# Kernel optimization log

Measured on AMD Instinct MI355X. Metric: run time of the kernel, lower is better.

Reference implementation:

```python
import jax, jax.numpy as jnp
import numpy as np

D_MODEL = 1024
N_HEADS = 16
N_GROUPS = 4
D_FF = 4096
N_EXPERTS = 8
TOP_K = 2
BATCH = 2
SEQ = 1024
D_K = D_MODEL // N_HEADS
HPG = N_HEADS // N_GROUPS
EPS = 1e-6


def rms_norm(x, w):
    rms = jnp.sqrt(jnp.mean(x * x, axis=-1, keepdims=True) + EPS)
    return x / rms * w


def rope(x):
    # RoPE over FULL d_model, halves concatenated (faithful to source quirk)
    d = x.shape[-1]
    half = d // 2
    theta = 1.0 / (10000.0 ** (jnp.arange(half, dtype=jnp.float32) / half))
    pos = jnp.arange(x.shape[1], dtype=jnp.float32)[:, None]  # [S,1]
    ang = pos * theta[None, :]                                 # [S,half]
    cos, sin = jnp.cos(ang), jnp.sin(ang)
    xe, xo = x[..., 0::2], x[..., 1::2]
    return jnp.concatenate([xe * cos - xo * sin, xe * sin + xo * cos], axis=-1)


def attention(x, Wq, Wk, Wv, Wo):
    B, S, _ = x.shape
    xr = rope(x)
    Q = (xr @ Wq).reshape(B, S, N_HEADS, D_K).transpose(0, 2, 1, 3)  # [B,H,S,dk]
    Q = Q.reshape(B, N_GROUPS, HPG, S, D_K)
    K = (xr @ Wk).reshape(B, S, N_GROUPS, D_K).transpose(0, 2, 1, 3)  # [B,G,S,dk]
    V = (xr @ Wv).reshape(B, S, N_GROUPS, D_K).transpose(0, 2, 1, 3)
    scores = jnp.einsum('bghsd,bgtd->bghst', Q, K) / jnp.sqrt(jnp.float32(D_K))
    mask = jnp.triu(jnp.full((S, S), -1e9, dtype=scores.dtype), k=1)
    attn = jax.nn.softmax(scores + mask, axis=-1)
    out = jnp.einsum('bghst,bgtd->bghsd', attn, V)            # [B,G,Hg,S,dv]
    out = out.reshape(B, N_HEADS, S, D_K).transpose(0, 2, 1, 3).reshape(B, S, D_MODEL)
    return out @ Wo


def moe(x, router_w, router_b, W1, b1, W2, b2, W3, b3):
    B, S, _ = x.shape
    logits = x @ router_w + router_b                          # [B,S,E]
    topv, topi = jax.lax.top_k(logits, TOP_K)                 # [B,S,K]
    topw = jax.nn.softmax(topv, axis=-1)                      # [B,S,K]
    # scatter top-k weights into dense [B,S,E] combine matrix
    onehot = jax.nn.one_hot(topi, N_EXPERTS, dtype=x.dtype)   # [B,S,K,E]
    comb = jnp.einsum('bsk,bske->bse', topw, onehot)          # [B,S,E]
    # dense all-expert SwiGLU (same math as per-token dispatch loop)
    h1 = jnp.einsum('bsd,edf->ebsf', x, W1) + b1[:, None, None, :]
    h2 = jnp.einsum('bsd,edf->ebsf', x, W2) + b2[:, None, None, :]
    h = h2 * jax.nn.silu(h1)
    eo = jnp.einsum('ebsf,efd->ebsd', h, W3) + b3[:, None, None, :]
    return jnp.einsum('bse,ebsd->bsd', comb, eo)


def setup_inputs() -> dict:
    key = jax.random.key(0)
    ks = jax.random.split(key, 16)
    s = 0.02
    return {
        'x': jax.random.normal(ks[0], (BATCH, SEQ, D_MODEL), dtype=jnp.float32),
        'norm1_w': jnp.ones((D_MODEL,), jnp.float32),
        'Wq': jax.random.normal(ks[1], (D_MODEL, D_MODEL), jnp.float32) * s,
        'Wk': jax.random.normal(ks[2], (D_MODEL, N_GROUPS * D_K), jnp.float32) * s,
        'Wv': jax.random.normal(ks[3], (D_MODEL, N_GROUPS * D_K), jnp.float32) * s,
        'Wo': jax.random.normal(ks[4], (D_MODEL, D_MODEL), jnp.float32) * s,
        'norm2_w': jnp.ones((D_MODEL,), jnp.float32),
        'router_w': jax.random.normal(ks[5], (D_MODEL, N_EXPERTS), jnp.float32) * s,
        'router_b': jnp.zeros((N_EXPERTS,), jnp.float32),
        'W1': jax.random.normal(ks[6], (N_EXPERTS, D_MODEL, D_FF), jnp.float32) * s,
        'b1': jnp.zeros((N_EXPERTS, D_FF), jnp.float32),
        'W2': jax.random.normal(ks[7], (N_EXPERTS, D_MODEL, D_FF), jnp.float32) * s,
        'b2': jnp.zeros((N_EXPERTS, D_FF), jnp.float32),
        'W3': jax.random.normal(ks[8], (N_EXPERTS, D_FF, D_MODEL), jnp.float32) * s,
        'b3': jnp.zeros((N_EXPERTS, D_MODEL), jnp.float32),
    }


def reference(x, norm1_w, Wq, Wk, Wv, Wo, norm2_w, router_w, router_b,
              W1, b1, W2, b2, W3, b3):
    h = x + attention(rms_norm(x, norm1_w), Wq, Wk, Wv, Wo)
    h = h + moe(rms_norm(h, norm2_w), router_w, router_b, W1, b1, W2, b2, W3, b3)
    return h
```

## Files before the change

kernel.cpp:

```cpp
#include <hip/hip_runtime.h>

#define D_MODEL 1024
#define N_HEADS 16
#define N_GROUPS 4
#define D_FF 4096
#define N_EXPERTS 8
#define BATCH 2
#define SEQ 1024
#define DK 64
#define NTOK (BATCH*SEQ)
#define KVD (N_GROUPS*DK)
#define QKVN (D_MODEL + 2*KVD)
#define APAD 72

typedef unsigned short u16;
typedef unsigned int u32;
typedef __attribute__((ext_vector_type(8))) short short8;
typedef __attribute__((ext_vector_type(8))) __bf16 bf16x8;
typedef __attribute__((ext_vector_type(4))) float floatx4;

__device__ __forceinline__ float bf2f(u16 s){ return __uint_as_float(((u32)s)<<16); }
__device__ __forceinline__ u16 f2bf(float f){
  u32 u = __float_as_uint(f);
  u += 0x7fffu + ((u>>16)&1u);
  return (u16)(u>>16);
}
__device__ __forceinline__ floatx4 mfma16(short8 a, short8 b, floatx4 c){
  return __builtin_amdgcn_mfma_f32_16x16x32_bf16(
      __builtin_bit_cast(bf16x8, a), __builtin_bit_cast(bf16x8, b), c, 0, 0, 0);
}
__device__ __forceinline__ void gload16(const u16* g, u16* l){
  __builtin_amdgcn_global_load_lds(
      (const __attribute__((address_space(1))) u32*)g,
      (__attribute__((address_space(3))) u32*)l, 16, 0, 0);
}

__global__ __launch_bounds__(256) void k_cvt_t(
    const float* __restrict__ src, u16* __restrict__ dst, int K, int N)
{
  size_t moff = (size_t)blockIdx.z * K * N;
  src += moff; dst += moff;
  int k0 = blockIdx.y*64, n0 = blockIdx.x*64;
  __shared__ __align__(16) u16 t[64*72];
  int tid = threadIdx.x;
  #pragma unroll
  for (int i=0;i<4;i++){
    int idx = i*256 + tid;
    int r = idx>>4;
    int c = (idx&15)*4;
    float4 v = *(const float4*)(src + (size_t)(k0+r)*N + n0 + c);
    t[(c+0)*72 + r] = f2bf(v.x);
    t[(c+1)*72 + r] = f2bf(v.y);
    t[(c+2)*72 + r] = f2bf(v.z);
    t[(c+3)*72 + r] = f2bf(v.w);
  }
  __syncthreads();
  #pragma unroll
  for (int i=0;i<2;i++){
    int idx = i*256 + tid;
    int n = idx>>3;
    int kc = (idx&7)*8;
    *(uint4*)(dst + (size_t)(n0+n)*K + k0 + kc) = *(const uint4*)&t[n*72 + kc];
  }
}

__global__ __launch_bounds__(256) void k_rmsnorm_rope(
    const float* __restrict__ x, const float* __restrict__ w, u16* __restrict__ xr)
{
  int tok = blockIdx.x;
  int s = tok & (SEQ-1);
  int tid = threadIdx.x;
  const float* xrow = x + (size_t)tok * D_MODEL;
  __shared__ float red[256];
  float4 v = ((const float4*)xrow)[tid];
  red[tid] = v.x*v.x + v.y*v.y + v.z*v.z + v.w*v.w;
  __syncthreads();
  for (int o=128;o>0;o>>=1){ if(tid<o) red[tid]+=red[tid+o]; __syncthreads(); }
  float inv = rsqrtf(red[0]*(1.0f/D_MODEL) + 1e-6f);
  u16* orow = xr + (size_t)tok * D_MODEL;
  #pragma unroll
  for (int ii=0; ii<2; ii++){
    int i = tid + ii*256;
    float2 p = ((const float2*)xrow)[i];
    float2 wp = ((const float2*)w)[i];
    float xe = p.x*inv*wp.x;
    float xo = p.y*inv*wp.y;
    float th = __expf(-(float)i * (9.210340371976184f/512.0f));
    float ang = (float)s * th;
    float c = cosf(ang), sn = sinf(ang);
    orow[i]       = f2bf(xe*c - xo*sn);
    orow[i+512]   = f2bf(xe*sn + xo*c);
  }
}

__global__ __launch_bounds__(256) void k_gemm_t(
    const u16* __restrict__ A, const u16* __restrict__ Bt,
    u16* __restrict__ C, int M, int N, int K)
{
  __shared__ __align__(16) u16 As[128*32];
  __shared__ __align__(16) u16 Bs[128*32];
  int tid = threadIdx.x;
  int wave = tid>>6, lane = tid&63, l15 = lane&15, q = lane>>4;
  int wm = wave>>1, wn = wave&1;
  int m0 = blockIdx.y*128, n0 = blockIdx.x*128;
  const u16* ap0 = A  + (size_t)(m0 + (tid>>2))*K + (tid&3)*8;
  const u16* ap1 = ap0 + (size_t)64*K;
  const u16* bp0 = Bt + (size_t)(n0 + (tid>>2))*K + (tid&3)*8;
  const u16* bp1 = bp0 + (size_t)64*K;
  u16* asb0 = As + wave*512;
  u16* asb1 = As + 2048 + wave*512;
  u16* bsb0 = Bs + wave*512;
  u16* bsb1 = Bs + 2048 + wave*512;
  floatx4 acc[4][4];
  #pragma unroll
  for (int i=0;i<4;i++)
    #pragma unroll
    for (int j=0;j<4;j++) acc[i][j] = (floatx4){0.f,0.f,0.f,0.f};
  for (int k0=0;k0<K;k0+=32){
    __syncthreads();
    gload16(ap0 + k0, asb0);
    gload16(ap1 + k0, asb1);
    gload16(bp0 + k0, bsb0);
    gload16(bp1 + k0, bsb1);
    __syncthreads();
    short8 af[4], bf[4];
    #pragma unroll
    for (int i=0;i<4;i++) af[i] = *(const short8*)&As[(wm*64 + i*16 + l15)*32 + q*8];
    #pragma unroll
    for (int i=0;i<4;i++) bf[i] = *(const short8*)&Bs[(wn*64 + i*16 + l15)*32 + q*8];
    #pragma unroll
    for (int mi=0;mi<4;mi++)
      #pragma unroll
      for (int ni=0;ni<4;ni++)
        acc[mi][ni] = mfma16(af[mi], bf[ni], acc[mi][ni]);
  }
  #pragma unroll
  for (int mi=0;mi<4;mi++)
    #pragma unroll
    for (int ni=0;ni<4;ni++)
      #pragma unroll
      for (int r=0;r<4;r++){
        int row = m0 + wm*64 + mi*16 + q*4 + r;
        int col = n0 + wn*64 + ni*16 + l15;
        C[(size_t)row*N + col] = f2bf(acc[mi][ni][r]);
      }
}

__global__ __launch_bounds__(256) void k_gemm_resid(
    const u16* __restrict__ A, const u16* __restrict__ Bt,
    const float* __restrict__ resid, float* __restrict__ hacc,
    float* __restrict__ out, int M, int N, int K)
{
  __shared__ __align__(16) u16 As[128*32];
  __shared__ __align__(16) u16 Bs[128*32];
  int tid = threadIdx.x;
  int wave = tid>>6, lane = tid&63, l15 = lane&15, q = lane>>4;
  int wm = wave>>1, wn = wave&1;
  int m0 = blockIdx.y*128, n0 = blockIdx.x*128;
  const u16* ap0 = A  + (size_t)(m0 + (tid>>2))*K + (tid&3)*8;
  const u16* ap1 = ap0 + (size_t)64*K;
  const u16* bp0 = Bt + (size_t)(n0 + (tid>>2))*K + (tid&3)*8;
  const u16* bp1 = bp0 + (size_t)64*K;
  u16* asb0 = As + wave*512;
  u16* asb1 = As + 2048 + wave*512;
  u16* bsb0 = Bs + wave*512;
  u16* bsb1 = Bs + 2048 + wave*512;
  floatx4 acc[4][4];
  #pragma unroll
  for (int i=0;i<4;i++)
    #pragma unroll
    for (int j=0;j<4;j++) acc[i][j] = (floatx4){0.f,0.f,0.f,0.f};
  for (int k0=0;k0<K;k0+=32){
    __syncthreads();
    gload16(ap0 + k0, asb0);
    gload16(ap1 + k0, asb1);
    gload16(bp0 + k0, bsb0);
    gload16(bp1 + k0, bsb1);
    __syncthreads();
    short8 af[4], bf[4];
    #pragma unroll
    for (int i=0;i<4;i++) af[i] = *(const short8*)&As[(wm*64 + i*16 + l15)*32 + q*8];
    #pragma unroll
    for (int i=0;i<4;i++) bf[i] = *(const short8*)&Bs[(wn*64 + i*16 + l15)*32 + q*8];
    #pragma unroll
    for (int mi=0;mi<4;mi++)
      #pragma unroll
      for (int ni=0;ni<4;ni++)
        acc[mi][ni] = mfma16(af[mi], bf[ni], acc[mi][ni]);
  }
  #pragma unroll
  for (int mi=0;mi<4;mi++)
    #pragma unroll
    for (int ni=0;ni<4;ni++)
      #pragma unroll
      for (int r=0;r<4;r++){
        int row = m0 + wm*64 + mi*16 + q*4 + r;
        int col = n0 + wn*64 + ni*16 + l15;
        size_t idx = (size_t)row*N + col;
        float v = acc[mi][ni][r] + resid[idx];
        hacc[idx] = v;
        out[idx]  = v;
      }
}

__global__ __launch_bounds__(256) void k_vtrans(
    const u16* __restrict__ qkv, u16* __restrict__ Vt)
{
  int st = blockIdx.x;
  int bg = blockIdx.y;
  int b = bg >> 2, g = bg & 3;
  int tid = threadIdx.x;
  __shared__ u16 tile[64*APAD];
  #pragma unroll
  for (int i=0;i<2;i++){
    int idx = i*256 + tid;
    int srow = idx >> 3, cch = (idx&7)*8;
    uint4 v = *(const uint4*)(qkv + (size_t)(b*SEQ + st*64 + srow)*QKVN
                              + D_MODEL + KVD + g*64 + cch);
    *(uint4*)&tile[srow*APAD + cch] = v;
  }
  __syncthreads();
  #pragma unroll
  for (int i=0;i<2;i++){
    int idx = i*256 + tid;
    int drow = idx >> 3, sch = (idx&7)*8;
    u16 tmp[8];
    #pragma unroll
    for (int j=0;j<8;j++) tmp[j] = tile[(sch+j)*APAD + drow];
    *(uint4*)(Vt + ((size_t)(bg*64 + drow))*SEQ + st*64 + sch) = *(uint4*)tmp;
  }
}

__global__ __launch_bounds__(256) void k_attn_flash(
    const u16* __restrict__ qkv, const u16* __restrict__ Vt, u16* __restrict__ O)
{
  int qt = blockIdx.x, h = blockIdx.y, b = blockIdx.z;
  int g = h >> 2;
  int tid = threadIdx.x, wave = tid>>6, lane = tid&63, l15 = lane&15, q = lane>>4;
  __shared__ u16 Ks[64*APAD];
  __shared__ u16 Vs[64*APAD];
  __shared__ u16 Ps[4*16*APAD];

  int qbase = qt*64;
  const u16* qrow = qkv + (size_t)(b*SEQ + qbase + wave*16 + l15)*QKVN + h*64;
  short8 qa0 = *(const short8*)(qrow + q*8);
  short8 qa1 = *(const short8*)(qrow + 32 + q*8);

  floatx4 Of[4];
  #pragma unroll
  for (int nt=0;nt<4;nt++) Of[nt] = (floatx4){0.f,0.f,0.f,0.f};
  float mrun[4], lrun[4];
  #pragma unroll
  for (int r=0;r<4;r++){ mrun[r] = -1e30f; lrun[r] = 0.f; }

  for (int t=0; t<=qt; ++t){
    int kbase = t*64;
    __syncthreads();
    #pragma unroll
    for (int i=0;i<2;i++){
      int idx = i*256 + tid;
      int row = idx >> 3, cch = (idx&7)*8;
      uint4 kv = *(const uint4*)(qkv + (size_t)(b*SEQ + kbase + row)*QKVN
                                 + D_MODEL + g*64 + cch);
      *(uint4*)&Ks[row*APAD + cch] = kv;
      uint4 vv = *(const uint4*)(Vt + ((size_t)((b*4+g)*64 + row))*SEQ + kbase + cch);
      *(uint4*)&Vs[row*APAD + cch] = vv;
    }
    __syncthreads();

    floatx4 Sf[4];
    #pragma unroll
    for (int jt=0;jt<4;jt++){
      short8 bf0 = *(const short8*)&Ks[(jt*16+l15)*APAD + q*8];
      short8 bf1 = *(const short8*)&Ks[(jt*16+l15)*APAD + 32 + q*8];
      Sf[jt] = mfma16(qa0, bf0, (floatx4){0.f,0.f,0.f,0.f});
      Sf[jt] = mfma16(qa1, bf1, Sf[jt]);
    }
    bool maskt = (t == qt);
    #pragma unroll
    for (int r=0;r<4;r++){
      float s0 = Sf[0][r]*0.125f, s1 = Sf[1][r]*0.125f,
            s2 = Sf[2][r]*0.125f, s3 = Sf[3][r]*0.125f;
      if (maskt){
        int qg = qbase + wave*16 + q*4 + r;
        if (kbase +      l15 > qg) s0 = -1e30f;
        if (kbase + 16 + l15 > qg) s1 = -1e30f;
        if (kbase + 32 + l15 > qg) s2 = -1e30f;
        if (kbase + 48 + l15 > qg) s3 = -1e30f;
      }
      float mx = fmaxf(fmaxf(s0,s1), fmaxf(s2,s3));
      #pragma unroll
      for (int o=1;o<16;o<<=1) mx = fmaxf(mx, __shfl_xor(mx, o, 64));
      float mc = fmaxf(mrun[r], mx);
      float alpha = __expf(mrun[r]-mc);
      float p0 = __expf(s0-mc), p1 = __expf(s1-mc), p2 = __expf(s2-mc), p3 = __expf(s3-mc);
      float rs = p0+p1+p2+p3;
      #pragma unroll
      for (int o=1;o<16;o<<=1) rs += __shfl_xor(rs, o, 64);
      lrun[r] = lrun[r]*alpha + rs;
      mrun[r] = mc;
      #pragma unroll
      for (int nt=0;nt<4;nt++) Of[nt][r] *= alpha;
      int prow = wave*16*APAD + (q*4+r)*APAD;
      Ps[prow +      l15] = f2bf(p0);
      Ps[prow + 16 + l15] = f2bf(p1);
      Ps[prow + 32 + l15] = f2bf(p2);
      Ps[prow + 48 + l15] = f2bf(p3);
    }
    #pragma unroll
    for (int ks=0;ks<2;ks++){
      short8 pa = *(const short8*)&Ps[wave*16*APAD + l15*APAD + ks*32 + q*8];
      #pragma unroll
      for (int nt=0;nt<4;nt++){
        short8 vb = *(const short8*)&Vs[(nt*16+l15)*APAD + ks*32 + q*8];
        Of[nt] = mfma16(pa, vb, Of[nt]);
      }
    }
  }
  #pragma unroll
  for (int r=0;r<4;r++){
    float linv = 1.0f / lrun[r];
    int row = b*SEQ + qbase + wave*16 + q*4 + r;
    #pragma unroll
    for (int nt=0;nt<4;nt++){
      O[(size_t)row*D_MODEL + h*64 + nt*16 + l15] = f2bf(Of[nt][r]*linv);
    }
  }
}

__global__ __launch_bounds__(256) void k_rmsnorm2(
    const float* __restrict__ hacc, const float* __restrict__ w, u16* __restrict__ hn)
{
  int tok = blockIdx.x, tid = threadIdx.x;
  float4 v = ((const float4*)(hacc + (size_t)tok*D_MODEL))[tid];
  __shared__ float red[256];
  red[tid] = v.x*v.x + v.y*v.y + v.z*v.z + v.w*v.w;
  __syncthreads();
  for (int o=128;o>0;o>>=1){ if(tid<o) red[tid]+=red[tid+o]; __syncthreads(); }
  float inv = rsqrtf(red[0]*(1.0f/D_MODEL) + 1e-6f);
  int i = tid*4;
  float4 wv = ((const float4*)w)[tid];
  u16* orow = hn + (size_t)tok*D_MODEL;
  orow[i+0] = f2bf(v.x*inv*wv.x);
  orow[i+1] = f2bf(v.y*inv*wv.y);
  orow[i+2] = f2bf(v.z*inv*wv.z);
  orow[i+3] = f2bf(v.w*inv*wv.w);
}

__global__ __launch_bounds__(64) void k_router(
    const float* __restrict__ hacc, const float* __restrict__ w2,
    const float* __restrict__ rw, const float* __restrict__ rb,
    int* __restrict__ topi, float* __restrict__ topw)
{
  int tok = blockIdx.x, lane = threadIdx.x;
  const float* xrow = hacc + (size_t)tok*D_MODEL;
  float ss = 0.f;
  #pragma unroll
  for (int ii=0; ii<4; ii++){
    float4 v = ((const float4*)xrow)[lane + ii*64];
    ss += v.x*v.x + v.y*v.y + v.z*v.z + v.w*v.w;
  }
  #pragma unroll
  for (int o=32;o>0;o>>=1) ss += __shfl_down(ss, o, 64);
  ss = __shfl(ss, 0, 64);
  float inv = rsqrtf(ss*(1.0f/D_MODEL) + 1e-6f);
  float accv[8] = {0.f,0.f,0.f,0.f,0.f,0.f,0.f,0.f};
  for (int d = lane; d < D_MODEL; d += 64){
    float xv = xrow[d]*inv*w2[d];
    float4 r0 = ((const float4*)(rw + (size_t)d*8))[0];
    float4 r1 = ((const float4*)(rw + (size_t)d*8))[1];
    accv[0] += xv*r0.x; accv[1] += xv*r0.y;
    accv[2] += xv*r0.z; accv[3] += xv*r0.w;
    accv[4] += xv*r1.x; accv[5] += xv*r1.y;
    accv[6] += xv*r1.z; accv[7] += xv*r1.w;
  }
  #pragma unroll
  for (int e=0;e<8;e++){
    #pragma unroll
    for (int o=32;o>0;o>>=1) accv[e] += __shfl_down(accv[e], o, 64);
  }
  if (lane==0){
    float lg[8];
    #pragma unroll
    for (int e=0;e<8;e++) lg[e] = accv[e] + rb[e];
    int i0=0; float v0=lg[0];
    for (int e=1;e<8;e++) if (lg[e]>v0){v0=lg[e]; i0=e;}
    int i1=-1; float v1=-1e30f;
    for (int e=0;e<8;e++) if (e!=i0 && lg[e]>v1){v1=lg[e]; i1=e;}
    float e1 = __expf(v1-v0);
    float wsum = 1.f + e1;
    topi[tok*2+0]=i0; topi[tok*2+1]=i1;
    topw[tok*2+0]=1.f/wsum; topw[tok*2+1]=e1/wsum;
  }
}

__global__ __launch_bounds__(256) void k_pack(
    const int* __restrict__ topi, const float* __restrict__ topw,
    int* __restrict__ off, int* __restrict__ perm, float* __restrict__ pw)
{
  __shared__ int cnt[8], cur[8], offs[9];
  int tid = threadIdx.x;
  if (tid<8) cnt[tid]=0;
  __syncthreads();
  for (int i=tid;i<NTOK*2;i+=256) atomicAdd(&cnt[topi[i]],1);
  __syncthreads();
  if (tid==0){
    int s=0;
    for (int e=0;e<8;e++){ offs[e]=s; s+=cnt[e]; }
    offs[8]=s;
    for (int e=0;e<9;e++) off[e]=offs[e];
  }
  __syncthreads();
  if (tid<8) cur[tid]=offs[tid];
  __syncthreads();
  for (int i=tid;i<NTOK*2;i+=256){
    int e = topi[i];
    int pos = atomicAdd(&cur[e],1);
    perm[pos] = i>>1;
    pw[pos]   = topw[i];
  }
}

__global__ __launch_bounds__(256) void k_moe1(
    const u16* __restrict__ hn,
    const u16* __restrict__ W1t, const float* __restrict__ b1,
    const u16* __restrict__ W2t, const float* __restrict__ b2,
    const int* __restrict__ off, const int* __restrict__ perm,
    u16* __restrict__ H)
{
  int e = blockIdx.z;
  int base = off[e], cnte = off[e+1]-base;
  int mt = blockIdx.y;
  if (mt*128 >= cnte) return;
  int n0 = blockIdx.x*64;
  __shared__ __align__(16) u16 As[128*32];
  __shared__ __align__(16) u16 B1s[64*32];
  __shared__ __align__(16) u16 B2s[64*32];
  int tid = threadIdx.x;
  int wave = tid>>6, lane = tid&63, l15 = lane&15, q = lane>>4;
  int wm = wave>>1, wn = wave&1;
  int r0 = mt*128 + (tid>>2), r1 = r0 + 64;
  int t0 = (r0 < cnte) ? perm[base+r0] : 0;
  int t1 = (r1 < cnte) ? perm[base+r1] : 0;
  const u16* ap0 = hn + (size_t)t0*D_MODEL + (tid&3)*8;
  const u16* ap1 = hn + (size_t)t1*D_MODEL + (tid&3)*8;
  const u16* b1p = W1t + (size_t)e*D_FF*D_MODEL + (size_t)(n0 + (tid>>2))*D_MODEL + (tid&3)*8;
  const u16* b2p = W2t + (size_t)e*D_FF*D_MODEL + (size_t)(n0 + (tid>>2))*D_MODEL + (tid&3)*8;
  u16* asb0 = As + wave*512;
  u16* asb1 = As + 2048 + wave*512;
  u16* b1sb = B1s + wave*512;
  u16* b2sb = B2s + wave*512;
  floatx4 acc1[4][2], acc2[4][2];
  #pragma unroll
  for (int i=0;i<4;i++)
    #pragma unroll
    for (int j=0;j<2;j++){ acc1[i][j]=(floatx4){0.f,0.f,0.f,0.f}; acc2[i][j]=(floatx4){0.f,0.f,0.f,0.f}; }
  for (int k0=0;k0<D_MODEL;k0+=32){
    __syncthreads();
    gload16(ap0 + k0, asb0);
    gload16(ap1 + k0, asb1);
    gload16(b1p + k0, b1sb);
    gload16(b2p + k0, b2sb);
    __syncthreads();
    short8 af[4], f1[2], f2[2];
    #pragma unroll
    for (int i=0;i<4;i++) af[i] = *(const short8*)&As[(wm*64 + i*16 + l15)*32 + q*8];
    #pragma unroll
    for (int i=0;i<2;i++){
      f1[i] = *(const short8*)&B1s[(wn*32 + i*16 + l15)*32 + q*8];
      f2[i] = *(const short8*)&B2s[(wn*32 + i*16 + l15)*32 + q*8];
    }
    #pragma unroll
    for (int mi=0;mi<4;mi++)
      #pragma unroll
      for (int ni=0;ni<2;ni++){
        acc1[mi][ni] = mfma16(af[mi], f1[ni], acc1[mi][ni]);
        acc2[mi][ni] = mfma16(af[mi], f2[ni], acc2[mi][ni]);
      }
  }
  #pragma unroll
  for (int mi=0;mi<4;mi++)
    #pragma unroll
    for (int ni=0;ni<2;ni++)
      #pragma unroll
      for (int r=0;r<4;r++){
        int rloc = wm*64 + mi*16 + q*4 + r;
        int grow = mt*128 + rloc;
        if (grow < cnte){
          int col = n0 + wn*32 + ni*16 + l15;
          float h1 = acc1[mi][ni][r] + b1[e*D_FF+col];
          float h2 = acc2[mi][ni][r] + b2[e*D_FF+col];
          float sil = h1 / (1.f + __expf(-h1));
          H[(size_t)(base + grow)*D_FF + col] = f2bf(h2*sil);
        }
      }
}

__global__ __launch_bounds__(256) void k_moe2(
    const u16* __restrict__ H, const u16* __restrict__ W3t, const float* __restrict__ b3,
    const int* __restrict__ off, const int* __restrict__ perm, const float* __restrict__ pw,
    float* __restrict__ out)
{
  int e = blockIdx.z;
  int base = off[e], cnte = off[e+1]-base;
  int mt = blockIdx.y;
  if (mt*128 >= cnte) return;
  int n0 = blockIdx.x*128;
  __shared__ __align__(16) u16 As[128*32];
  __shared__ __align__(16) u16 Bs[128*32];
  int tid = threadIdx.x;
  int wave = tid>>6, lane = tid&63, l15 = lane&15, q = lane>>4;
  int wm = wave>>1, wn = wave&1;
  const u16* ap0 = H + (size_t)(base + mt*128 + (tid>>2))*D_FF + (tid&3)*8;
  const u16* ap1 = ap0 + (size_t)64*D_FF;
  const u16* bp0 = W3t + (size_t)e*D_MODEL*D_FF + (size_t)(n0 + (tid>>2))*D_FF + (tid&3)*8;
  const u16* bp1 = bp0 + (size_t)64*D_FF;
  u16* asb0 = As + wave*512;
  u16* asb1 = As + 2048 + wave*512;
  u16* bsb0 = Bs + wave*512;
  u16* bsb1 = Bs + 2048 + wave*512;
  floatx4 acc[4][4];
  #pragma unroll
  for (int i=0;i<4;i++)
    #pragma unroll
    for (int j=0;j<4;j++) acc[i][j] = (floatx4){0.f,0.f,0.f,0.f};
  for (int k0=0;k0<D_FF;k0+=32){
    __syncthreads();
    gload16(ap0 + k0, asb0);
    gload16(ap1 + k0, asb1);
    gload16(bp0 + k0, bsb0);
    gload16(bp1 + k0, bsb1);
    __syncthreads();
    short8 af[4], bf[4];
    #pragma unroll
    for (int i=0;i<4;i++) af[i] = *(const short8*)&As[(wm*64 + i*16 + l15)*32 + q*8];
    #pragma unroll
    for (int i=0;i<4;i++) bf[i] = *(const short8*)&Bs[(wn*64 + i*16 + l15)*32 + q*8];
    #pragma unroll
    for (int mi=0;mi<4;mi++)
      #pragma unroll
      for (int ni=0;ni<4;ni++)
        acc[mi][ni] = mfma16(af[mi], bf[ni], acc[mi][ni]);
  }
  #pragma unroll
  for (int mi=0;mi<4;mi++)
    #pragma unroll
    for (int ni=0;ni<4;ni++)
      #pragma unroll
      for (int r=0;r<4;r++){
        int grow = mt*128 + wm*64 + mi*16 + q*4 + r;
        if (grow < cnte){
          int col = n0 + wn*64 + ni*16 + l15;
          int tok = perm[base+grow];
          float wgt = pw[base+grow];
          float val = acc[mi][ni][r] + b3[e*D_MODEL+col];
          atomicAdd(out + (size_t)tok*D_MODEL + col, wgt*val);
        }
      }
}

extern "C" void kernel_launch(void* const* d_in, const int* in_sizes, int n_in,
                              void* d_out, int out_size, void* d_ws, size_t ws_size,
                              hipStream_t stream)
{
  const float* x   = (const float*)d_in[0];
  const float* n1w = (const float*)d_in[1];
  const float* Wq  = (const float*)d_in[2];
  const float* Wk  = (const float*)d_in[3];
  const float* Wv  = (const float*)d_in[4];
  const float* Wo  = (const float*)d_in[5];
  const float* n2w = (const float*)d_in[6];
  const float* rw  = (const float*)d_in[7];
  const float* rb  = (const float*)d_in[8];
  const float* W1  = (const float*)d_in[9];
  const float* b1  = (const float*)d_in[10];
  const float* W2  = (const float*)d_in[11];
  const float* b2  = (const float*)d_in[12];
  const float* W3  = (const float*)d_in[13];
  const float* b3  = (const float*)d_in[14];
  float* out = (float*)d_out;

  char* p = (char*)d_ws;
  auto alloc = [&](size_t bytes)->char*{
    char* r = p; p += (bytes + 255) & ~(size_t)255; return r;
  };
  u16*   xr   = (u16*)  alloc((size_t)NTOK*D_MODEL*2);
  u16*   qkv  = (u16*)  alloc((size_t)NTOK*QKVN*2);
  u16*   Vt   = (u16*)  alloc((size_t)NTOK*KVD*2);
  u16*   attn = (u16*)  alloc((size_t)NTOK*D_MODEL*2);
  u16*   hn   = (u16*)  alloc((size_t)NTOK*D_MODEL*2);
  float* acc  = (float*)alloc((size_t)NTOK*D_MODEL*4);
  int*   topi = (int*)  alloc((size_t)NTOK*2*4);
  float* topw = (float*)alloc((size_t)NTOK*2*4);
  int*   off  = (int*)  alloc(64);
  int*   perm = (int*)  alloc((size_t)NTOK*2*4);
  float* pw   = (float*)alloc((size_t)NTOK*2*4);
  u16*   H    = (u16*)  alloc((size_t)NTOK*2*D_FF*2);
  u16*   Wqkvt= (u16*)  alloc((size_t)QKVN*D_MODEL*2);
  u16*   Wot  = (u16*)  alloc((size_t)D_MODEL*D_MODEL*2);
  u16*   W1t  = (u16*)  alloc((size_t)N_EXPERTS*D_MODEL*D_FF*2);
  u16*   W2t  = (u16*)  alloc((size_t)N_EXPERTS*D_MODEL*D_FF*2);
  u16*   W3t  = (u16*)  alloc((size_t)N_EXPERTS*D_FF*D_MODEL*2);

  k_cvt_t<<<dim3(D_MODEL/64, D_MODEL/64, 1), 256, 0, stream>>>(Wq, Wqkvt, D_MODEL, D_MODEL);
  k_cvt_t<<<dim3(KVD/64,     D_MODEL/64, 1), 256, 0, stream>>>(Wk, Wqkvt + (size_t)D_MODEL*D_MODEL, D_MODEL, KVD);
  k_cvt_t<<<dim3(KVD/64,     D_MODEL/64, 1), 256, 0, stream>>>(Wv, Wqkvt + (size_t)(D_MODEL+KVD)*D_MODEL, D_MODEL, KVD);
  k_cvt_t<<<dim3(D_MODEL/64, D_MODEL/64, 1), 256, 0, stream>>>(Wo, Wot, D_MODEL, D_MODEL);
  k_cvt_t<<<dim3(D_FF/64,    D_MODEL/64, N_EXPERTS), 256, 0, stream>>>(W1, W1t, D_MODEL, D_FF);
  k_cvt_t<<<dim3(D_FF/64,    D_MODEL/64, N_EXPERTS), 256, 0, stream>>>(W2, W2t, D_MODEL, D_FF);
  k_cvt_t<<<dim3(D_MODEL/64, D_FF/64,    N_EXPERTS), 256, 0, stream>>>(W3, W3t, D_FF, D_MODEL);

  k_rmsnorm_rope<<<NTOK, 256, 0, stream>>>(x, n1w, xr);
  k_gemm_t<<<dim3(QKVN/128, NTOK/128), 256, 0, stream>>>(xr, Wqkvt, qkv, NTOK, QKVN, D_MODEL);
  k_vtrans<<<dim3(SEQ/64, BATCH*N_GROUPS), 256, 0, stream>>>(qkv, Vt);
  k_attn_flash<<<dim3(SEQ/64, N_HEADS, BATCH), 256, 0, stream>>>(qkv, Vt, attn);
  k_gemm_resid<<<dim3(D_MODEL/128, NTOK/128), 256, 0, stream>>>(attn, Wot, x, acc, out, NTOK, D_MODEL, D_MODEL);
  k_rmsnorm2<<<NTOK, 256, 0, stream>>>(acc, n2w, hn);
  k_router<<<NTOK, 64, 0, stream>>>(acc, n2w, rw, rb, topi, topw);
  k_pack<<<1, 256, 0, stream>>>(topi, topw, off, perm, pw);
  k_moe1<<<dim3(D_FF/64,    32, N_EXPERTS), 256, 0, stream>>>(hn, W1t, b1, W2t, b2, off, perm, H);
  k_moe2<<<dim3(D_MODEL/128, 32, N_EXPERTS), 256, 0, stream>>>(H, W3t, b3, off, perm, pw, out);
}
```

Baseline: 843.2 us.

## Double-buffer LDS in GEMM kernels, shrink M tiles, split-K the MoE down projection

Adds a two-stage LDS ping-pong to the QKV, output-projection and both MoE GEMMs, so the global load for the next K slice is issued before the MFMAs on the current slice and one barrier per iteration is dropped. The dense GEMMs and moe2 move from 128-row to 64-row M tiles to launch more blocks, and moe2 splits K in two, with both halves accumulating through the existing atomics and the bias added only once. The cost is twice the shared memory per block, which may lower occupancy, less reuse per tile, and twice as many atomic adds into the output in moe2.

```diff
diff --git a/kernel.cpp b/kernel.cpp
--- a/kernel.cpp
+++ b/kernel.cpp
@@ -97,50 +97,50 @@
     const u16* __restrict__ A, const u16* __restrict__ Bt,
     u16* __restrict__ C, int M, int N, int K)
 {
-  __shared__ __align__(16) u16 As[128*32];
-  __shared__ __align__(16) u16 Bs[128*32];
+  __shared__ __align__(16) u16 As[2][64*32];
+  __shared__ __align__(16) u16 Bs[2][128*32];
   int tid = threadIdx.x;
   int wave = tid>>6, lane = tid&63, l15 = lane&15, q = lane>>4;
   int wm = wave>>1, wn = wave&1;
-  int m0 = blockIdx.y*128, n0 = blockIdx.x*128;
-  const u16* ap0 = A  + (size_t)(m0 + (tid>>2))*K + (tid&3)*8;
-  const u16* ap1 = ap0 + (size_t)64*K;
+  int m0 = blockIdx.y*64, n0 = blockIdx.x*128;
+  const u16* ap  = A  + (size_t)(m0 + (tid>>2))*K + (tid&3)*8;
   const u16* bp0 = Bt + (size_t)(n0 + (tid>>2))*K + (tid&3)*8;
   const u16* bp1 = bp0 + (size_t)64*K;
-  u16* asb0 = As + wave*512;
-  u16* asb1 = As + 2048 + wave*512;
-  u16* bsb0 = Bs + wave*512;
-  u16* bsb1 = Bs + 2048 + wave*512;
-  floatx4 acc[4][4];
-  #pragma unroll
-  for (int i=0;i<4;i++)
+  auto stage = [&](int buf, int k){
+    gload16(ap  + k, &As[buf][wave*512]);
+    gload16(bp0 + k, &Bs[buf][wave*512]);
+    gload16(bp1 + k, &Bs[buf][2048 + wave*512]);
+  };
+  floatx4 acc[2][4];
+  #pragma unroll
+  for (int i=0;i<2;i++)
     #pragma unroll
     for (int j=0;j<4;j++) acc[i][j] = (floatx4){0.f,0.f,0.f,0.f};
-  for (int k0=0;k0<K;k0+=32){
-    __syncthreads();
-    gload16(ap0 + k0, asb0);
-    gload16(ap1 + k0, asb1);
-    gload16(bp0 + k0, bsb0);
-    gload16(bp1 + k0, bsb1);
-    __syncthreads();
-    short8 af[4], bf[4];
-    #pragma unroll
-    for (int i=0;i<4;i++) af[i] = *(const short8*)&As[(wm*64 + i*16 + l15)*32 + q*8];
-    #pragma unroll
-    for (int i=0;i<4;i++) bf[i] = *(const short8*)&Bs[(wn*64 + i*16 + l15)*32 + q*8];
-    #pragma unroll
-    for (int mi=0;mi<4;mi++)
+  int NS = K/32, cur = 0;
+  stage(0, 0);
+  __syncthreads();
+  for (int ks=0; ks<NS; ++ks){
+    if (ks+1 < NS) stage(cur^1, (ks+1)*32);
+    short8 af[2], bf[4];
+    #pragma unroll
+    for (int i=0;i<2;i++) af[i] = *(const short8*)&As[cur][(wm*32 + i*16 + l15)*32 + q*8];
+    #pragma unroll
+    for (int i=0;i<4;i++) bf[i] = *(const short8*)&Bs[cur][(wn*64 + i*16 + l15)*32 + q*8];
+    #pragma unroll
+    for (int mi=0;mi<2;mi++)
       #pragma unroll
       for (int ni=0;ni<4;ni++)
         acc[mi][ni] = mfma16(af[mi], bf[ni], acc[mi][ni]);
-  }
-  #pragma unroll
-  for (int mi=0;mi<4;mi++)
+    __syncthreads();
+    cur ^= 1;
+  }
+  #pragma unroll
+  for (int mi=0;mi<2;mi++)
     #pragma unroll
     for (int ni=0;ni<4;ni++)
       #pragma unroll
       for (int r=0;r<4;r++){
-        int row = m0 + wm*64 + mi*16 + q*4 + r;
+        int row = m0 + wm*32 + mi*16 + q*4 + r;
         int col = n0 + wn*64 + ni*16 + l15;
         C[(size_t)row*N + col] = f2bf(acc[mi][ni][r]);
       }
@@ -151,50 +151,50 @@
     const float* __restrict__ resid, float* __restrict__ hacc,
     float* __restrict__ out, int M, int N, int K)
 {
-  __shared__ __align__(16) u16 As[128*32];
-  __shared__ __align__(16) u16 Bs[128*32];
+  __shared__ __align__(16) u16 As[2][64*32];
+  __shared__ __align__(16) u16 Bs[2][128*32];
   int tid = threadIdx.x;
   int wave = tid>>6, lane = tid&63, l15 = lane&15, q = lane>>4;
   int wm = wave>>1, wn = wave&1;
-  int m0 = blockIdx.y*128, n0 = blockIdx.x*128;
-  const u16* ap0 = A  + (size_t)(m0 + (tid>>2))*K + (tid&3)*8;
-  const u16* ap1 = ap0 + (size_t)64*K;
+  int m0 = blockIdx.y*64, n0 = blockIdx.x*128;
+  const u16* ap  = A  + (size_t)(m0 + (tid>>2))*K + (tid&3)*8;
   const u16* bp0 = Bt + (size_t)(n0 + (tid>>2))*K + (tid&3)*8;
   const u16* bp1 = bp0 + (size_t)64*K;
-  u16* asb0 = As + wave*512;
-  u16* asb1 = As + 2048 + wave*512;
-  u16* bsb0 = Bs + wave*512;
-  u16* bsb1 = Bs + 2048 + wave*512;
-  floatx4 acc[4][4];
-  #pragma unroll
-  for (int i=0;i<4;i++)
+  auto stage = [&](int buf, int k){
+    gload16(ap  + k, &As[buf][wave*512]);
+    gload16(bp0 + k, &Bs[buf][wave*512]);
+    gload16(bp1 + k, &Bs[buf][2048 + wave*512]);
+  };
+  floatx4 acc[2][4];
+  #pragma unroll
+  for (int i=0;i<2;i++)
     #pragma unroll
     for (int j=0;j<4;j++) acc[i][j] = (floatx4){0.f,0.f,0.f,0.f};
-  for (int k0=0;k0<K;k0+=32){
-    __syncthreads();
-    gload16(ap0 + k0, asb0);
-    gload16(ap1 + k0, asb1);
-    gload16(bp0 + k0, bsb0);
-    gload16(bp1 + k0, bsb1);
-    __syncthreads();
-    short8 af[4], bf[4];
-    #pragma unroll
-    for (int i=0;i<4;i++) af[i] = *(const short8*)&As[(wm*64 + i*16 + l15)*32 + q*8];
-    #pragma unroll
-    for (int i=0;i<4;i++) bf[i] = *(const short8*)&Bs[(wn*64 + i*16 + l15)*32 + q*8];
-    #pragma unroll
-    for (int mi=0;mi<4;mi++)
+  int NS = K/32, cur = 0;
+  stage(0, 0);
+  __syncthreads();
+  for (int ks=0; ks<NS; ++ks){
+    if (ks+1 < NS) stage(cur^1, (ks+1)*32);
+    short8 af[2], bf[4];
+    #pragma unroll
+    for (int i=0;i<2;i++) af[i] = *(const short8*)&As[cur][(wm*32 + i*16 + l15)*32 + q*8];
+    #pragma unroll
+    for (int i=0;i<4;i++) bf[i] = *(const short8*)&Bs[cur][(wn*64 + i*16 + l15)*32 + q*8];
+    #pragma unroll
+    for (int mi=0;mi<2;mi++)
       #pragma unroll
       for (int ni=0;ni<4;ni++)
         acc[mi][ni] = mfma16(af[mi], bf[ni], acc[mi][ni]);
-  }
-  #pragma unroll
-  for (int mi=0;mi<4;mi++)
+    __syncthreads();
+    cur ^= 1;
+  }
+  #pragma unroll
+  for (int mi=0;mi<2;mi++)
     #pragma unroll
     for (int ni=0;ni<4;ni++)
       #pragma unroll
       for (int r=0;r<4;r++){
-        int row = m0 + wm*64 + mi*16 + q*4 + r;
+        int row = m0 + wm*32 + mi*16 + q*4 + r;
         int col = n0 + wn*64 + ni*16 + l15;
         size_t idx = (size_t)row*N + col;
         float v = acc[mi][ni][r] + resid[idx];
@@ -433,9 +433,9 @@
   int mt = blockIdx.y;
   if (mt*128 >= cnte) return;
   int n0 = blockIdx.x*64;
-  __shared__ __align__(16) u16 As[128*32];
-  __shared__ __align__(16) u16 B1s[64*32];
-  __shared__ __align__(16) u16 B2s[64*32];
+  __shared__ __align__(16) u16 As[2][128*32];
+  __shared__ __align__(16) u16 B1s[2][64*32];
+  __shared__ __align__(16) u16 B2s[2][64*32];
   int tid = threadIdx.x;
   int wave = tid>>6, lane = tid&63, l15 = lane&15, q = lane>>4;
   int wm = wave>>1, wn = wave&1;
@@ -446,29 +446,29 @@
   const u16* ap1 = hn + (size_t)t1*D_MODEL + (tid&3)*8;
   const u16* b1p = W1t + (size_t)e*D_FF*D_MODEL + (size_t)(n0 + (tid>>2))*D_MODEL + (tid&3)*8;
   const u16* b2p = W2t + (size_t)e*D_FF*D_MODEL + (size_t)(n0 + (tid>>2))*D_MODEL + (tid&3)*8;
-  u16* asb0 = As + wave*512;
-  u16* asb1 = As + 2048 + wave*512;
-  u16* b1sb = B1s + wave*512;
-  u16* b2sb = B2s + wave*512;
+  auto stage = [&](int buf, int k){
+    gload16(ap0 + k, &As[buf][wave*512]);
+    gload16(ap1 + k, &As[buf][2048 + wave*512]);
+    gload16(b1p + k, &B1s[buf][wave*512]);
+    gload16(b2p + k, &B2s[buf][wave*512]);
+  };
   floatx4 acc1[4][2], acc2[4][2];
   #pragma unroll
   for (int i=0;i<4;i++)
     #pragma unroll
     for (int j=0;j<2;j++){ acc1[i][j]=(floatx4){0.f,0.f,0.f,0.f}; acc2[i][j]=(floatx4){0.f,0.f,0.f,0.f}; }
-  for (int k0=0;k0<D_MODEL;k0+=32){
-    __syncthreads();
-    gload16(ap0 + k0, asb0);
-    gload16(ap1 + k0, asb1);
-    gload16(b1p + k0, b1sb);
-    gload16(b2p + k0, b2sb);
-    __syncthreads();
+  int cur = 0;
+  stage(0, 0);
+  __syncthreads();
+  for (int ks=0; ks<D_MODEL/32; ++ks){
+    if (ks+1 < D_MODEL/32) stage(cur^1, (ks+1)*32);
     short8 af[4], f1[2], f2[2];
     #pragma unroll
-    for (int i=0;i<4;i++) af[i] = *(const short8*)&As[(wm*64 + i*16 + l15)*32 + q*8];
+    for (int i=0;i<4;i++) af[i] = *(const short8*)&As[cur][(wm*64 + i*16 + l15)*32 + q*8];
     #pragma unroll
     for (int i=0;i<2;i++){
-      f1[i] = *(const short8*)&B1s[(wn*32 + i*16 + l15)*32 + q*8];
-      f2[i] = *(const short8*)&B2s[(wn*32 + i*16 + l15)*32 + q*8];
+      f1[i] = *(const short8*)&B1s[cur][(wn*32 + i*16 + l15)*32 + q*8];
+      f2[i] = *(const short8*)&B2s[cur][(wn*32 + i*16 + l15)*32 + q*8];
     }
     #pragma unroll
     for (int mi=0;mi<4;mi++)
@@ -477,6 +477,8 @@
         acc1[mi][ni] = mfma16(af[mi], f1[ni], acc1[mi][ni]);
         acc2[mi][ni] = mfma16(af[mi], f2[ni], acc2[mi][ni]);
       }
+    __syncthreads();
+    cur ^= 1;
   }
   #pragma unroll
   for (int mi=0;mi<4;mi++)
@@ -503,57 +505,58 @@
 {
   int e = blockIdx.z;
   int base = off[e], cnte = off[e+1]-base;
-  int mt = blockIdx.y;
-  if (mt*128 >= cnte) return;
+  int mt = blockIdx.y >> 1;
+  int ksp = blockIdx.y & 1;
+  if (mt*64 >= cnte) return;
   int n0 = blockIdx.x*128;
-  __shared__ __align__(16) u16 As[128*32];
-  __shared__ __align__(16) u16 Bs[128*32];
+  __shared__ __align__(16) u16 As[2][64*32];
+  __shared__ __align__(16) u16 Bs[2][128*32];
   int tid = threadIdx.x;
   int wave = tid>>6, lane = tid&63, l15 = lane&15, q = lane>>4;
   int wm = wave>>1, wn = wave&1;
-  const u16* ap0 = H + (size_t)(base + mt*128 + (tid>>2))*D_FF + (tid&3)*8;
-  const u16* ap1 = ap0 + (size_t)64*D_FF;
-  const u16* bp0 = W3t + (size_t)e*D_MODEL*D_FF + (size_t)(n0 + (tid>>2))*D_FF + (tid&3)*8;
+  const u16* ap  = H + (size_t)(base + mt*64 + (tid>>2))*D_FF + ksp*2048 + (tid&3)*8;
+  const u16* bp0 = W3t + (size_t)e*D_MODEL*D_FF + (size_t)(n0 + (tid>>2))*D_FF + ksp*2048 + (tid&3)*8;
   const u16* bp1 = bp0 + (size_t)64*D_FF;
-  u16* asb0 = As + wave*512;
-  u16* asb1 = As + 2048 + wave*512;
-  u16* bsb0 = Bs + wave*512;
-  u16* bsb1 = Bs + 2048 + wave*512;
-  floatx4 acc[4][4];
-  #pragma unroll
-  for (int i=0;i<4;i++)
+  auto stage = [&](int buf, int k){
+    gload16(ap  + k, &As[buf][wave*512]);
+    gload16(bp0 + k, &Bs[buf][wave*512]);
+    gload16(bp1 + k, &Bs[buf][2048 + wave*512]);
+  };
+  floatx4 acc[2][4];
+  #pragma unroll
+  for (int i=0;i<2;i++)
     #pragma unroll
     for (int j=0;j<4;j++) acc[i][j] = (floatx4){0.f,0.f,0.f,0.f};
-  for (int k0=0;k0<D_FF;k0+=32){
-    __syncthreads();
-    gload16(ap0 + k0, asb0);
-    gload16(ap1 + k0, asb1);
-    gload16(bp0 + k0, bsb0);
-    gload16(bp1 + k0, bsb1);
-    __syncthreads();
-    short8 af[4], bf[4];
-    #pragma unroll
-    for (int i=0;i<4;i++) af[i] = *(const short8*)&As[(wm*64 + i*16 + l15)*32 + q*8];
-    #pragma unroll
-    for (int i=0;i<4;i++) bf[i] = *(const short8*)&Bs[(wn*64 + i*16 + l15)*32 + q*8];
-    #pragma unroll
-    for (int mi=0;mi<4;mi++)
+  int cur = 0;
+  stage(0, 0);
+  __syncthreads();
+  for (int ks=0; ks<64; ++ks){
+    if (ks+1 < 64) stage(cur^1, (ks+1)*32);
+    short8 af[2], bf[4];
+    #pragma unroll
+    for (int i=0;i<2;i++) af[i] = *(const short8*)&As[cur][(wm*32 + i*16 + l15)*32 + q*8];
+    #pragma unroll
+    for (int i=0;i<4;i++) bf[i] = *(const short8*)&Bs[cur][(wn*64 + i*16 + l15)*32 + q*8];
+    #pragma unroll
+    for (int mi=0;mi<2;mi++)
       #pragma unroll
       for (int ni=0;ni<4;ni++)
         acc[mi][ni] = mfma16(af[mi], bf[ni], acc[mi][ni]);
-  }
-  #pragma unroll
-  for (int mi=0;mi<4;mi++)
+    __syncthreads();
+    cur ^= 1;
+  }
+  #pragma unroll
+  for (int mi=0;mi<2;mi++)
     #pragma unroll
     for (int ni=0;ni<4;ni++)
       #pragma unroll
       for (int r=0;r<4;r++){
-        int grow = mt*128 + wm*64 + mi*16 + q*4 + r;
+        int grow = mt*64 + wm*32 + mi*16 + q*4 + r;
         if (grow < cnte){
           int col = n0 + wn*64 + ni*16 + l15;
           int tok = perm[base+grow];
           float wgt = pw[base+grow];
-          float val = acc[mi][ni][r] + b3[e*D_MODEL+col];
+          float val = acc[mi][ni][r] + (ksp==0 ? b3[e*D_MODEL+col] : 0.f);
           atomicAdd(out + (size_t)tok*D_MODEL + col, wgt*val);
         }
       }
@@ -611,13 +614,13 @@
   k_cvt_t<<<dim3(D_MODEL/64, D_FF/64,    N_EXPERTS), 256, 0, stream>>>(W3, W3t, D_FF, D_MODEL);
 
   k_rmsnorm_rope<<<NTOK, 256, 0, stream>>>(x, n1w, xr);
-  k_gemm_t<<<dim3(QKVN/128, NTOK/128), 256, 0, stream>>>(xr, Wqkvt, qkv, NTOK, QKVN, D_MODEL);
+  k_gemm_t<<<dim3(QKVN/128, NTOK/64), 256, 0, stream>>>(xr, Wqkvt, qkv, NTOK, QKVN, D_MODEL);
   k_vtrans<<<dim3(SEQ/64, BATCH*N_GROUPS), 256, 0, stream>>>(qkv, Vt);
   k_attn_flash<<<dim3(SEQ/64, N_HEADS, BATCH), 256, 0, stream>>>(qkv, Vt, attn);
-  k_gemm_resid<<<dim3(D_MODEL/128, NTOK/128), 256, 0, stream>>>(attn, Wot, x, acc, out, NTOK, D_MODEL, D_MODEL);
+  k_gemm_resid<<<dim3(D_MODEL/128, NTOK/64), 256, 0, stream>>>(attn, Wot, x, acc, out, NTOK, D_MODEL, D_MODEL);
   k_rmsnorm2<<<NTOK, 256, 0, stream>>>(acc, n2w, hn);
   k_router<<<NTOK, 64, 0, stream>>>(acc, n2w, rw, rb, topi, topw);
   k_pack<<<1, 256, 0, stream>>>(topi, topw, off, perm, pw);
-  k_moe1<<<dim3(D_FF/64,    32, N_EXPERTS), 256, 0, stream>>>(hn, W1t, b1, W2t, b2, off, perm, H);
-  k_moe2<<<dim3(D_MODEL/128, 32, N_EXPERTS), 256, 0, stream>>>(H, W3t, b3, off, perm, pw, out);
-}
+  k_moe1<<<dim3(D_FF/64,     32, N_EXPERTS), 256, 0, stream>>>(hn, W1t, b1, W2t, b2, off, perm, H);
+  k_moe2<<<dim3(D_MODEL/128, 128, N_EXPERTS), 256, 0, stream>>>(H, W3t, b3, off, perm, pw, out);
+}
```

After: 786.8 us. 6.7% less time.
